# Optimization experiments

Hardware: AMD Instinct MI355X
Metric: run time of the kernel (lower is better)

## Reference

```python
import jax, jax.numpy as jnp
import numpy as np

B, S, D = 4, 2048, 1024
N_HEAD = 16
HEAD_DIM = D // N_HEAD


def setup_inputs() -> dict:
    key = jax.random.key(0)
    k1, k2, k3 = jax.random.split(key, 3)
    std = 0.02
    return {
        "x": jax.random.normal(k1, (B, S, D), dtype=jnp.float32),
        "c_attn_w": jax.random.normal(k2, (D, 3 * D), dtype=jnp.float32) * std,
        "c_attn_b": jnp.zeros((3 * D,), dtype=jnp.float32),
        "c_proj_w": jax.random.normal(k3, (D, D), dtype=jnp.float32) * std,
        "c_proj_b": jnp.zeros((D,), dtype=jnp.float32),
    }


def _split_heads(t):
    # [B, S, D] -> [B, H, S, hd]
    b, s, d = t.shape
    return t.reshape(b, s, N_HEAD, d // N_HEAD).transpose(0, 2, 1, 3)


def reference(x, c_attn_w, c_attn_b, c_proj_w, c_proj_b):
    # fused QKV projection (TFConv1D = x @ w + b)
    qkv = x @ c_attn_w + c_attn_b                      # [B, S, 3D]
    q, k, v = jnp.split(qkv, 3, axis=2)
    q, k, v = _split_heads(q), _split_heads(k), _split_heads(v)  # [B, H, S, hd]

    # scaled scores
    w = jnp.einsum('bhqd,bhkd->bhqk', q, k)
    w = w / jnp.sqrt(jnp.asarray(HEAD_DIM, w.dtype))

    # causal mask via multiplicative trick: i >= j - ns + nd (nd == ns == S)
    nd = ns = S
    i = jnp.arange(nd)[:, None]
    j = jnp.arange(ns)[None, :]
    b = (i >= j - ns + nd).astype(w.dtype)[None, None]  # [1,1,nd,ns]
    w = w * b - 10000.0 * (1.0 - b)

    w = jax.nn.softmax(w, axis=-1)
    a = jnp.einsum('bhqk,bhkd->bhqd', w, v)            # [B, H, S, hd]

    # merge heads: [B, H, S, hd] -> [B, S, D]
    a = a.transpose(0, 2, 1, 3).reshape(x.shape[0], x.shape[1], -1)
    a = a @ c_proj_w + c_proj_b
    return a
```

## Files before the change

### kernel.cpp

```cpp
#include <hip/hip_runtime.h>
#include <hip/hip_bf16.h>

typedef unsigned short ushort_t;
typedef __attribute__((ext_vector_type(8))) short short8;
typedef __attribute__((ext_vector_type(4))) float floatx4;

#define LOG2E 1.4426950408889634f

__device__ __forceinline__ unsigned short f2bf(float f) {
    unsigned u = __float_as_uint(f);
    u += 0x7FFF + ((u >> 16) & 1);
    return (unsigned short)(u >> 16);
}

__device__ __forceinline__ void async_ld16(const void* gptr, void* lptr) {
    typedef const __attribute__((address_space(1))) unsigned int TG;
    typedef __attribute__((address_space(3))) unsigned int TL;
    __builtin_amdgcn_global_load_lds((TG*)(unsigned long long)gptr,
                                     (TL*)(unsigned)(unsigned long long)lptr,
                                     16, 0, 0);
}

__global__ __launch_bounds__(256) void prep_kernel(const float* __restrict__ x,
                                                   const float* __restrict__ wqkv,
                                                   const float* __restrict__ wproj,
                                                   ushort_t* __restrict__ xb,
                                                   ushort_t* __restrict__ wqkvT,
                                                   ushort_t* __restrict__ wprojT) {
    __shared__ float t[32][33];
    int bx = blockIdx.x;
    if (bx < 8192) {
        int i = bx * 256 + threadIdx.x;
        float4 v = ((const float4*)x)[i];
        unsigned long long r = (unsigned long long)f2bf(v.x)
                             | ((unsigned long long)f2bf(v.y) << 16)
                             | ((unsigned long long)f2bf(v.z) << 32)
                             | ((unsigned long long)f2bf(v.w) << 48);
        ((unsigned long long*)xb)[i] = r;
        return;
    }
    const float* in; ushort_t* out; int R, C, bidx;
    if (bx < 8192 + 3072) { in = wqkv; out = wqkvT; R = 1024; C = 3072; bidx = bx - 8192; }
    else                  { in = wproj; out = wprojT; R = 1024; C = 1024; bidx = bx - 11264; }
    int nbc = C >> 5;
    int bc = bidx % nbc, br = bidx / nbc;
    int tx = threadIdx.x & 31, ty = threadIdx.x >> 5;
    int r0 = br << 5, c0 = bc << 5;
#pragma unroll
    for (int j = 0; j < 4; ++j)
        t[ty + j * 8][tx] = in[(size_t)(r0 + ty + j * 8) * C + c0 + tx];
    __syncthreads();
#pragma unroll
    for (int j = 0; j < 4; ++j)
        out[(size_t)(c0 + ty + j * 8) * R + r0 + tx] = f2bf(t[tx][ty + j * 8]);
}

__global__ __launch_bounds__(1024) void gemm_qkv_kernel(const ushort_t* __restrict__ A,
                                                        const ushort_t* __restrict__ Bt,
                                                        const float* __restrict__ bias,
                                                        ushort_t* __restrict__ qbuf,
                                                        ushort_t* __restrict__ kbuf,
                                                        ushort_t* __restrict__ vtbuf) {
    extern __shared__ __align__(16) ushort_t lds[];

    int bid = blockIdx.x;
    int wg = (bid & 7) * 96 + (bid >> 3);
    int bm = wg & 63, bn = wg >> 6;
    int m0 = bm << 7, n0 = bn << 8;

    int tid = threadIdx.x;
    int wave = tid >> 6, lane = tid & 63;
    int c = lane & 15, g = lane >> 4;
    int wm = wave >> 2, wn = wave & 3;

    int row0 = tid >> 3;
    int sch  = (tid & 7) ^ (row0 & 7);
    size_t aoff = (size_t)(m0 + row0) * 1024 + sch * 8;
    size_t boff = (size_t)(n0 + row0) * 1024 + sch * 8;

    int co0 = (g * 8) ^ ((c & 7) << 3);
    int co1 = co0 ^ 32;

    floatx4 acc[2][4];
    short8 a[2][2], bf[2][2], bg[2][2];
#pragma unroll
    for (int i2 = 0; i2 < 2; ++i2)
#pragma unroll
        for (int j2 = 0; j2 < 4; ++j2) { floatx4 z = {0.f,0.f,0.f,0.f}; acc[i2][j2] = z; }

    auto stA = [&](int t, int buf) {
        async_ld16(A + aoff + (size_t)t * 64, lds + buf * 8192 + tid * 8);
    };
    auto stB = [&](int t, int buf) {
        const ushort_t* s = Bt + boff + (size_t)t * 64;
        ushort_t* d = lds + 16384 + buf * 16384 + tid * 8;
        async_ld16(s, d);
        async_ld16(s + 131072, d + 8192);
    };
    auto ld_a = [&](int buf) {
#pragma unroll
        for (int mi = 0; mi < 2; ++mi) {
            int ro = buf * 8192 + (wm * 32 + mi * 16 + c) * 64;
            a[mi][0] = *(const short8*)&lds[ro + co0];
            a[mi][1] = *(const short8*)&lds[ro + co1];
        }
    };
    auto ld_b = [&](int buf, int q, short8 (&bb)[2][2]) {
#pragma unroll
        for (int nii = 0; nii < 2; ++nii) {
            int ro = 16384 + buf * 16384 + (wn * 64 + (q * 2 + nii) * 16 + c) * 64;
            bb[nii][0] = *(const short8*)&lds[ro + co0];
            bb[nii][1] = *(const short8*)&lds[ro + co1];
        }
    };
    auto phase_mm = [&](int q, short8 (&bb)[2][2]) {
        asm volatile("s_barrier" ::: "memory");
        asm volatile("s_waitcnt lgkmcnt(0)" ::: "memory");
        __builtin_amdgcn_s_setprio(1);
#pragma unroll
        for (int mi = 0; mi < 2; ++mi)
#pragma unroll
            for (int nii = 0; nii < 2; ++nii)
#pragma unroll
                for (int ks = 0; ks < 2; ++ks)
                    acc[mi][q * 2 + nii] =
                        __builtin_amdgcn_mfma_f32_16x16x32_bf16(
                            a[mi][ks], bb[nii][ks], acc[mi][q * 2 + nii], 0, 0, 0);
        __builtin_amdgcn_s_setprio(0);
        asm volatile("s_barrier" ::: "memory");
    };

    stA(0, 0); stB(0, 0);
    stA(1, 1); stB(1, 1);
    asm volatile("s_waitcnt vmcnt(3)" ::: "memory");
    asm volatile("s_barrier" ::: "memory");

#pragma unroll 1
    for (int i = 0; i < 14; ++i) {
        int buf = i & 1;
        ld_a(buf); ld_b(buf, 0, bf);
        stA(i + 2, buf);
        phase_mm(0, bf);
        ld_b(buf, 1, bg);
        stB(i + 2, buf);
        asm volatile("s_waitcnt vmcnt(3)" ::: "memory");
        phase_mm(1, bg);
    }
    ld_a(0); ld_b(0, 0, bf);
    phase_mm(0, bf);
    ld_b(0, 1, bg);
    asm volatile("s_waitcnt vmcnt(0)" ::: "memory");
    phase_mm(1, bg);
    ld_a(1); ld_b(1, 0, bf);
    phase_mm(0, bf);
    ld_b(1, 1, bg);
    phase_mm(1, bg);

    int sec = n0 >> 10;
    int h0 = (n0 & 1023) >> 6;
    int b  = m0 >> 11, sbase = m0 & 2047;
    int bh0 = b * 16 + h0;
    float bv[4];
#pragma unroll
    for (int ni = 0; ni < 4; ++ni) bv[ni] = bias[n0 + wn * 64 + ni * 16 + c];

    __syncthreads();

    if (sec < 2) {
        float scl = (sec == 0) ? (0.125f * LOG2E) : 1.0f;
#pragma unroll
        for (int mi = 0; mi < 2; ++mi)
#pragma unroll
            for (int ni = 0; ni < 4; ++ni)
#pragma unroll
                for (int r = 0; r < 4; ++r) {
                    int row = wm * 32 + mi * 16 + g * 4 + r;
                    lds[wn * 9216 + row * 72 + ni * 16 + c] =
                        f2bf((acc[mi][ni][r] + bv[ni]) * scl);
                }
        __syncthreads();
        ushort_t* dstbase = (sec == 0 ? qbuf : kbuf);
        int head = tid >> 8, row = (tid >> 1) & 127, half = tid & 1;
        const ushort_t* src = &lds[head * 9216 + row * 72 + half * 32];
        ushort_t* dst = dstbase + (size_t)(bh0 + head) * 131072
                      + (size_t)(sbase + row) * 64 + half * 32;
#pragma unroll
        for (int j = 0; j < 4; ++j)
            *(short8*)(dst + j * 8) = *(const short8*)(src + j * 8);
    } else {
#pragma unroll
        for (int mi = 0; mi < 2; ++mi)
#pragma unroll
            for (int ni = 0; ni < 4; ++ni) {
                int d = ni * 16 + c;
                int s0 = wm * 32 + mi * 16 + g * 4;
                unsigned long long pk =
                      (unsigned long long)f2bf(acc[mi][ni][0] + bv[ni])
                    | ((unsigned long long)f2bf(acc[mi][ni][1] + bv[ni]) << 16)
                    | ((unsigned long long)f2bf(acc[mi][ni][2] + bv[ni]) << 32)
                    | ((unsigned long long)f2bf(acc[mi][ni][3] + bv[ni]) << 48);
                *(unsigned long long*)&lds[wn * 8704 + d * 136 + s0] = pk;
            }
        __syncthreads();
        int head = tid >> 8, dd = (tid >> 2) & 63, sq = tid & 3;
        const ushort_t* src = &lds[head * 8704 + dd * 136 + sq * 32];
        ushort_t* dst = vtbuf + (size_t)(bh0 + head) * 131072
                      + (size_t)dd * 2048 + sbase + sq * 32;
#pragma unroll
        for (int j = 0; j < 4; ++j)
            *(short8*)(dst + j * 8) = *(const short8*)(src + j * 8);
    }
}

__global__ __launch_bounds__(256, 6) void attn_kernel(const ushort_t* __restrict__ qb_,
                                                      const ushort_t* __restrict__ kb_,
                                                      const ushort_t* __restrict__ vtb_,
                                                      ushort_t* __restrict__ aout) {
    __shared__ __align__(16) ushort_t Ks[64 * 68];
    __shared__ __align__(16) ushort_t Vs[64 * 68];
    __shared__ __align__(16) ushort_t Ps[4][16 * 68];
    int bx = blockIdx.x;
    int qb = 31 - (bx >> 6);
    int bhix = bx & 63;
    int b = bhix >> 4, h = bhix & 15;
    int q0 = qb << 6;
    int tid = threadIdx.x, wave = tid >> 6, lane = tid & 63;
    int c = lane & 15, g = lane >> 4;
    size_t bh = (size_t)(b * 16 + h);

    const ushort_t* Qp = qb_ + (bh * 2048 + q0) * 64;
    const ushort_t* Kp = kb_ + bh * 131072;
    const ushort_t* Vp = vtb_ + bh * 131072;

    int qr = wave * 16 + c;
    short8 qf0 = *(const short8*)(Qp + qr * 64 + g * 8);
    short8 qf1 = *(const short8*)(Qp + qr * 64 + 32 + g * 8);

    short8 vones;
#pragma unroll
    for (int j = 0; j < 8; ++j) vones[j] = (short)0x3F80;

    floatx4 o_acc[4];
    floatx4 lacc = {0.f, 0.f, 0.f, 0.f};
#pragma unroll
    for (int nt = 0; nt < 4; ++nt) { floatx4 z = {0.f,0.f,0.f,0.f}; o_acc[nt] = z; }

    short8 kreg[2], vreg[2];
#pragma unroll
    for (int it = 0; it < 2; ++it) {
        int idx = it * 256 + tid;
        kreg[it] = *(const short8*)(Kp + idx * 8);
        vreg[it] = *(const short8*)(Vp + (idx >> 3) * 2048 + (idx & 7) * 8);
    }

    int qg = q0 + wave * 16 + c;
    for (int kt = 0; kt <= qb; ++kt) {
        int kt0 = kt << 6;
        __syncthreads();
#pragma unroll
        for (int it = 0; it < 2; ++it) {
            int idx = it * 256 + tid;
            *(short8*)&Ks[(idx >> 3) * 68 + (idx & 7) * 8] = kreg[it];
            *(short8*)&Vs[(idx >> 3) * 68 + (idx & 7) * 8] = vreg[it];
        }
        __syncthreads();
        if (kt < qb) {
            int s0 = (kt + 1) << 6;
#pragma unroll
            for (int it = 0; it < 2; ++it) {
                int idx = it * 256 + tid;
                kreg[it] = *(const short8*)(Kp + s0 * 64 + idx * 8);
                vreg[it] = *(const short8*)(Vp + (idx >> 3) * 2048 + s0 + (idx & 7) * 8);
            }
        }
        bool diag = (kt == qb);

#pragma unroll
        for (int nt = 0; nt < 4; ++nt) {
            short8 kf0 = *(const short8*)&Ks[(nt * 16 + c) * 68 + g * 8];
            short8 kf1 = *(const short8*)&Ks[(nt * 16 + c) * 68 + 32 + g * 8];
            floatx4 z = {0.f, 0.f, 0.f, 0.f};
            z = __builtin_amdgcn_mfma_f32_16x16x32_bf16(kf0, qf0, z, 0, 0, 0);
            z = __builtin_amdgcn_mfma_f32_16x16x32_bf16(kf1, qf1, z, 0, 0, 0);

            int kpb = kt0 + nt * 16 + g * 4;
            float p[4];
#pragma unroll
            for (int r = 0; r < 4; ++r) {
                float s = z[r];
                if (diag) s = (kpb + r > qg) ? -1e30f : s;
                p[r] = exp2f(s);
            }
            union { unsigned long long u; __hip_bfloat162 h2[2]; } pk;
            pk.h2[0] = __float22bfloat162_rn(make_float2(p[0], p[1]));
            pk.h2[1] = __float22bfloat162_rn(make_float2(p[2], p[3]));
            *(unsigned long long*)&Ps[wave][c * 68 + nt * 16 + g * 4] = pk.u;
        }

#pragma unroll
        for (int ks = 0; ks < 2; ++ks) {
            short8 pf = *(const short8*)&Ps[wave][c * 68 + ks * 32 + g * 8];
            lacc = __builtin_amdgcn_mfma_f32_16x16x32_bf16(pf, vones, lacc, 0, 0, 0);
#pragma unroll
            for (int nt = 0; nt < 4; ++nt) {
                short8 vf = *(const short8*)&Vs[(nt * 16 + c) * 68 + ks * 32 + g * 8];
                o_acc[nt] = __builtin_amdgcn_mfma_f32_16x16x32_bf16(pf, vf, o_acc[nt], 0, 0, 0);
            }
        }
    }

    float inv[4];
#pragma unroll
    for (int r = 0; r < 4; ++r)
        inv[r] = 1.0f / lacc[r];
#pragma unroll
    for (int nt = 0; nt < 4; ++nt)
#pragma unroll
        for (int r = 0; r < 4; ++r) {
            int q = q0 + wave * 16 + g * 4 + r;
            aout[(size_t)(b * 2048 + q) * 1024 + h * 64 + nt * 16 + c] =
                f2bf(o_acc[nt][r] * inv[r]);
        }
}

__global__ __launch_bounds__(256) void gemm_proj_kernel(const ushort_t* __restrict__ A,
                                                        const ushort_t* __restrict__ Bt,
                                                        const float* __restrict__ bias,
                                                        float* __restrict__ Cout) {
    const int K = 1024, N = 1024, nbn = 8;
    __shared__ __align__(16) ushort_t As[128 * 32];
    __shared__ __align__(16) ushort_t Bs[128 * 32];
    int bm = blockIdx.x / nbn, bn = blockIdx.x % nbn;
    int m0 = bm << 7, n0 = bn << 7;
    int tid = threadIdx.x;
    int wave = tid >> 6, lane = tid & 63;
    int c = lane & 15, g = lane >> 4;
    int m_off = (wave & 1) << 6, n_off = (wave >> 1) << 6;
    int ldrow = lane >> 2;
    int ldk   = (lane & 3) << 3;

    floatx4 acc[4][4];
#pragma unroll
    for (int mi = 0; mi < 4; ++mi)
#pragma unroll
        for (int ni = 0; ni < 4; ++ni) {
            floatx4 z = {0.f, 0.f, 0.f, 0.f};
            acc[mi][ni] = z;
        }

    for (int kk = 0; kk < K; kk += 32) {
        __syncthreads();
#pragma unroll
        for (int j = 0; j < 2; ++j) {
            int chunk = wave * 2 + j;
            async_ld16(A  + (size_t)(m0 + chunk * 16 + ldrow) * K + kk + ldk, &As[chunk * 512]);
            async_ld16(Bt + (size_t)(n0 + chunk * 16 + ldrow) * K + kk + ldk, &Bs[chunk * 512]);
        }
        __syncthreads();
        short8 bf[4];
#pragma unroll
        for (int ni = 0; ni < 4; ++ni)
            bf[ni] = *(const short8*)&Bs[(n_off + ni * 16 + c) * 32 + g * 8];
#pragma unroll
        for (int mi = 0; mi < 4; ++mi) {
            short8 af = *(const short8*)&As[(m_off + mi * 16 + c) * 32 + g * 8];
#pragma unroll
            for (int ni = 0; ni < 4; ++ni)
                acc[mi][ni] = __builtin_amdgcn_mfma_f32_16x16x32_bf16(af, bf[ni], acc[mi][ni], 0, 0, 0);
        }
    }

    float bv[4];
#pragma unroll
    for (int ni = 0; ni < 4; ++ni) bv[ni] = bias[n0 + n_off + ni * 16 + c];
#pragma unroll
    for (int mi = 0; mi < 4; ++mi)
#pragma unroll
        for (int ni = 0; ni < 4; ++ni)
#pragma unroll
            for (int r = 0; r < 4; ++r) {
                int row = m0 + m_off + mi * 16 + g * 4 + r;
                int col = n0 + n_off + ni * 16 + c;
                Cout[(size_t)row * N + col] = acc[mi][ni][r] + bv[ni];
            }
}

extern "C" void kernel_launch(void* const* d_in, const int* in_sizes, int n_in,
                              void* d_out, int out_size, void* d_ws, size_t ws_size,
                              hipStream_t stream) {
    const float* x        = (const float*)d_in[0];
    const float* c_attn_w = (const float*)d_in[1];
    const float* c_attn_b = (const float*)d_in[2];
    const float* c_proj_w = (const float*)d_in[3];
    const float* c_proj_b = (const float*)d_in[4];
    float* out = (float*)d_out;

    char* ws = (char*)d_ws;
    ushort_t* xb     = (ushort_t*)(ws);
    ushort_t* wqkvT  = (ushort_t*)(ws + 16777216);
    ushort_t* wprojT = (ushort_t*)(ws + 23068672);
    ushort_t* qbuf   = (ushort_t*)(ws + 25165824);
    ushort_t* kbuf   = (ushort_t*)(ws + 41943040);
    ushort_t* vtbuf  = (ushort_t*)(ws + 58720256);

    static bool s_attr_set = false;
    if (!s_attr_set) {
        (void)hipFuncSetAttribute(reinterpret_cast<const void*>(gemm_qkv_kernel),
                                  hipFuncAttributeMaxDynamicSharedMemorySize, 98304);
        s_attr_set = true;
    }

    prep_kernel<<<12288, 256, 0, stream>>>(x, c_attn_w, c_proj_w, xb, wqkvT, wprojT);
    gemm_qkv_kernel<<<768, 1024, 98304, stream>>>(xb, wqkvT, c_attn_b, qbuf, kbuf, vtbuf);
    attn_kernel<<<2048, 256, 0, stream>>>(qbuf, kbuf, vtbuf, xb);
    gemm_proj_kernel<<<64 * 8, 256, 0, stream>>>(xb, wprojT, c_proj_b, out);
}
```

Measured before the change: 279.2 us.

## Widen QKV GEMM tiles to 128x384 and port proj GEMM to pipelined 1024-thread kernel

The QKV GEMM moves from 128x256 tiles with 768 blocks to 128x384 tiles with 512 blocks, giving each wave a 64x48 sub-tile. The epilogue now handles a block spanning up to six heads and mixed Q/K/V sections, writing them out per head. The output projection GEMM is replaced with the same double-buffered, swizzled, async-LDS 1024-thread design using 256x128 tiles. The aim is more reuse of each operand load per MFMA and better latency hiding in the projection. The cost is more LDS per block (128KB) and fewer blocks, which may reduce occupancy or leave CUs unevenly loaded.

Result: faster. 262.6 us (-5.9%).

```diff
diff --git a/kernel.cpp b/kernel.cpp
--- a/kernel.cpp
+++ b/kernel.cpp
@@ -64,14 +64,14 @@
     extern __shared__ __align__(16) ushort_t lds[];
 
     int bid = blockIdx.x;
-    int wg = (bid & 7) * 96 + (bid >> 3);
+    int wg = (bid & 7) * 64 + (bid >> 3);
     int bm = wg & 63, bn = wg >> 6;
-    int m0 = bm << 7, n0 = bn << 8;
+    int m0 = bm << 7, n0 = bn * 384;
 
     int tid = threadIdx.x;
     int wave = tid >> 6, lane = tid & 63;
     int c = lane & 15, g = lane >> 4;
-    int wm = wave >> 2, wn = wave & 3;
+    int wm = wave >> 3, wn = wave & 7;
 
     int row0 = tid >> 3;
     int sch  = (tid & 7) ^ (row0 & 7);
@@ -81,134 +81,139 @@
     int co0 = (g * 8) ^ ((c & 7) << 3);
     int co1 = co0 ^ 32;
 
-    floatx4 acc[2][4];
-    short8 a[2][2], bf[2][2], bg[2][2];
-#pragma unroll
-    for (int i2 = 0; i2 < 2; ++i2)
-#pragma unroll
-        for (int j2 = 0; j2 < 4; ++j2) { floatx4 z = {0.f,0.f,0.f,0.f}; acc[i2][j2] = z; }
+    floatx4 acc[4][3];
+    short8 a[4][2], bb[2];
+#pragma unroll
+    for (int i2 = 0; i2 < 4; ++i2)
+#pragma unroll
+        for (int j2 = 0; j2 < 3; ++j2) { floatx4 z = {0.f,0.f,0.f,0.f}; acc[i2][j2] = z; }
 
     auto stA = [&](int t, int buf) {
         async_ld16(A + aoff + (size_t)t * 64, lds + buf * 8192 + tid * 8);
     };
     auto stB = [&](int t, int buf) {
         const ushort_t* s = Bt + boff + (size_t)t * 64;
-        ushort_t* d = lds + 16384 + buf * 16384 + tid * 8;
+        ushort_t* d = lds + 16384 + buf * 24576 + tid * 8;
         async_ld16(s, d);
         async_ld16(s + 131072, d + 8192);
+        async_ld16(s + 262144, d + 16384);
     };
     auto ld_a = [&](int buf) {
 #pragma unroll
-        for (int mi = 0; mi < 2; ++mi) {
-            int ro = buf * 8192 + (wm * 32 + mi * 16 + c) * 64;
+        for (int mi = 0; mi < 4; ++mi) {
+            int ro = buf * 8192 + (wm * 64 + mi * 16 + c) * 64;
             a[mi][0] = *(const short8*)&lds[ro + co0];
             a[mi][1] = *(const short8*)&lds[ro + co1];
         }
     };
-    auto ld_b = [&](int buf, int q, short8 (&bb)[2][2]) {
-#pragma unroll
-        for (int nii = 0; nii < 2; ++nii) {
-            int ro = 16384 + buf * 16384 + (wn * 64 + (q * 2 + nii) * 16 + c) * 64;
-            bb[nii][0] = *(const short8*)&lds[ro + co0];
-            bb[nii][1] = *(const short8*)&lds[ro + co1];
-        }
-    };
-    auto phase_mm = [&](int q, short8 (&bb)[2][2]) {
+    auto ld_b = [&](int buf, int nii) {
+        int ro = 16384 + buf * 24576 + (wn * 48 + nii * 16 + c) * 64;
+        bb[0] = *(const short8*)&lds[ro + co0];
+        bb[1] = *(const short8*)&lds[ro + co1];
+    };
+    auto mm = [&](int nii) {
         asm volatile("s_barrier" ::: "memory");
         asm volatile("s_waitcnt lgkmcnt(0)" ::: "memory");
         __builtin_amdgcn_s_setprio(1);
 #pragma unroll
-        for (int mi = 0; mi < 2; ++mi)
-#pragma unroll
-            for (int nii = 0; nii < 2; ++nii)
-#pragma unroll
-                for (int ks = 0; ks < 2; ++ks)
-                    acc[mi][q * 2 + nii] =
-                        __builtin_amdgcn_mfma_f32_16x16x32_bf16(
-                            a[mi][ks], bb[nii][ks], acc[mi][q * 2 + nii], 0, 0, 0);
+        for (int mi = 0; mi < 4; ++mi)
+#pragma unroll
+            for (int ks = 0; ks < 2; ++ks)
+                acc[mi][nii] = __builtin_amdgcn_mfma_f32_16x16x32_bf16(
+                    a[mi][ks], bb[ks], acc[mi][nii], 0, 0, 0);
         __builtin_amdgcn_s_setprio(0);
         asm volatile("s_barrier" ::: "memory");
     };
 
     stA(0, 0); stB(0, 0);
     stA(1, 1); stB(1, 1);
-    asm volatile("s_waitcnt vmcnt(3)" ::: "memory");
+    asm volatile("s_waitcnt vmcnt(4)" ::: "memory");
     asm volatile("s_barrier" ::: "memory");
 
 #pragma unroll 1
-    for (int i = 0; i < 14; ++i) {
-        int buf = i & 1;
-        ld_a(buf); ld_b(buf, 0, bf);
-        stA(i + 2, buf);
-        phase_mm(0, bf);
-        ld_b(buf, 1, bg);
-        stB(i + 2, buf);
-        asm volatile("s_waitcnt vmcnt(3)" ::: "memory");
-        phase_mm(1, bg);
-    }
-    ld_a(0); ld_b(0, 0, bf);
-    phase_mm(0, bf);
-    ld_b(0, 1, bg);
+    for (int t = 0; t < 14; ++t) {
+        int buf = t & 1;
+        ld_a(buf); ld_b(buf, 0);
+        mm(0);
+        ld_b(buf, 1);
+        mm(1);
+        ld_b(buf, 2);
+        stA(t + 2, buf); stB(t + 2, buf);
+        asm volatile("s_waitcnt vmcnt(4)" ::: "memory");
+        mm(2);
+    }
+    ld_a(0); ld_b(0, 0);
+    mm(0);
+    ld_b(0, 1);
+    mm(1);
+    ld_b(0, 2);
     asm volatile("s_waitcnt vmcnt(0)" ::: "memory");
-    phase_mm(1, bg);
-    ld_a(1); ld_b(1, 0, bf);
-    phase_mm(0, bf);
-    ld_b(1, 1, bg);
-    phase_mm(1, bg);
-
-    int sec = n0 >> 10;
-    int h0 = (n0 & 1023) >> 6;
-    int b  = m0 >> 11, sbase = m0 & 2047;
-    int bh0 = b * 16 + h0;
-    float bv[4];
-#pragma unroll
-    for (int ni = 0; ni < 4; ++ni) bv[ni] = bias[n0 + wn * 64 + ni * 16 + c];
+    mm(2);
+    ld_a(1); ld_b(1, 0);
+    mm(0);
+    ld_b(1, 1);
+    mm(1);
+    ld_b(1, 2);
+    mm(2);
+
+    int b = m0 >> 11, sbase = m0 & 2047;
+    float bv[3], scl[3];
+    int headf[3], cinh[3], secf[3];
+#pragma unroll
+    for (int nii = 0; nii < 3; ++nii) {
+        int cb = wn * 48 + nii * 16;
+        bv[nii]   = bias[n0 + cb + c];
+        headf[nii] = cb >> 6;
+        cinh[nii]  = (cb & 63) + c;
+        secf[nii]  = (n0 + cb) >> 10;
+        scl[nii]   = (secf[nii] == 0) ? (0.125f * LOG2E) : 1.0f;
+    }
 
     __syncthreads();
 
-    if (sec < 2) {
-        float scl = (sec == 0) ? (0.125f * LOG2E) : 1.0f;
-#pragma unroll
-        for (int mi = 0; mi < 2; ++mi)
-#pragma unroll
-            for (int ni = 0; ni < 4; ++ni)
+#pragma unroll
+    for (int nii = 0; nii < 3; ++nii) {
+        if (secf[nii] < 2) {
+#pragma unroll
+            for (int mi = 0; mi < 4; ++mi)
 #pragma unroll
                 for (int r = 0; r < 4; ++r) {
-                    int row = wm * 32 + mi * 16 + g * 4 + r;
-                    lds[wn * 9216 + row * 72 + ni * 16 + c] =
-                        f2bf((acc[mi][ni][r] + bv[ni]) * scl);
+                    int row = wm * 64 + mi * 16 + g * 4 + r;
+                    lds[headf[nii] * 9216 + row * 72 + cinh[nii]] =
+                        f2bf((acc[mi][nii][r] + bv[nii]) * scl[nii]);
                 }
-        __syncthreads();
-        ushort_t* dstbase = (sec == 0 ? qbuf : kbuf);
-        int head = tid >> 8, row = (tid >> 1) & 127, half = tid & 1;
-        const ushort_t* src = &lds[head * 9216 + row * 72 + half * 32];
-        ushort_t* dst = dstbase + (size_t)(bh0 + head) * 131072
-                      + (size_t)(sbase + row) * 64 + half * 32;
-#pragma unroll
-        for (int j = 0; j < 4; ++j)
-            *(short8*)(dst + j * 8) = *(const short8*)(src + j * 8);
-    } else {
-#pragma unroll
-        for (int mi = 0; mi < 2; ++mi)
-#pragma unroll
-            for (int ni = 0; ni < 4; ++ni) {
-                int d = ni * 16 + c;
-                int s0 = wm * 32 + mi * 16 + g * 4;
+        } else {
+#pragma unroll
+            for (int mi = 0; mi < 4; ++mi) {
+                int d = cinh[nii];
+                int s0 = wm * 64 + mi * 16 + g * 4;
                 unsigned long long pk =
-                      (unsigned long long)f2bf(acc[mi][ni][0] + bv[ni])
-                    | ((unsigned long long)f2bf(acc[mi][ni][1] + bv[ni]) << 16)
-                    | ((unsigned long long)f2bf(acc[mi][ni][2] + bv[ni]) << 32)
-                    | ((unsigned long long)f2bf(acc[mi][ni][3] + bv[ni]) << 48);
-                *(unsigned long long*)&lds[wn * 8704 + d * 136 + s0] = pk;
+                      (unsigned long long)f2bf(acc[mi][nii][0] + bv[nii])
+                    | ((unsigned long long)f2bf(acc[mi][nii][1] + bv[nii]) << 16)
+                    | ((unsigned long long)f2bf(acc[mi][nii][2] + bv[nii]) << 32)
+                    | ((unsigned long long)f2bf(acc[mi][nii][3] + bv[nii]) << 48);
+                *(unsigned long long*)&lds[headf[nii] * 9216 + d * 136 + s0] = pk;
             }
-        __syncthreads();
-        int head = tid >> 8, dd = (tid >> 2) & 63, sq = tid & 3;
-        const ushort_t* src = &lds[head * 8704 + dd * 136 + sq * 32];
-        ushort_t* dst = vtbuf + (size_t)(bh0 + head) * 131072
-                      + (size_t)dd * 2048 + sbase + sq * 32;
-#pragma unroll
-        for (int j = 0; j < 4; ++j)
-            *(short8*)(dst + j * 8) = *(const short8*)(src + j * 8);
+        }
+    }
+    __syncthreads();
+
+#pragma unroll 1
+    for (int hl = 0; hl < 6; ++hl) {
+        int colg = n0 + hl * 64;
+        int sech = colg >> 10;
+        int hg = (colg & 1023) >> 6;
+        size_t bh = (size_t)(b * 16 + hg);
+        if (sech < 2) {
+            int row = tid >> 3, ch = tid & 7;
+            ushort_t* dst = (sech == 0 ? qbuf : kbuf) + bh * 131072
+                          + (size_t)(sbase + row) * 64 + ch * 8;
+            *(short8*)dst = *(const short8*)&lds[hl * 9216 + row * 72 + ch * 8];
+        } else {
+            int d = tid >> 4, sq = tid & 15;
+            ushort_t* dst = vtbuf + bh * 131072 + (size_t)d * 2048 + sbase + sq * 8;
+            *(short8*)dst = *(const short8*)&lds[hl * 9216 + d * 136 + sq * 8];
+        }
     }
 }
 
@@ -323,65 +328,110 @@
         }
 }
 
-__global__ __launch_bounds__(256) void gemm_proj_kernel(const ushort_t* __restrict__ A,
-                                                        const ushort_t* __restrict__ Bt,
-                                                        const float* __restrict__ bias,
-                                                        float* __restrict__ Cout) {
-    const int K = 1024, N = 1024, nbn = 8;
-    __shared__ __align__(16) ushort_t As[128 * 32];
-    __shared__ __align__(16) ushort_t Bs[128 * 32];
-    int bm = blockIdx.x / nbn, bn = blockIdx.x % nbn;
-    int m0 = bm << 7, n0 = bn << 7;
+__global__ __launch_bounds__(1024) void gemm_proj_kernel(const ushort_t* __restrict__ A,
+                                                         const ushort_t* __restrict__ Bt,
+                                                         const float* __restrict__ bias,
+                                                         float* __restrict__ Cout) {
+    extern __shared__ __align__(16) ushort_t lds[];
+
+    int bid = blockIdx.x;
+    int wg = (bid & 7) * 32 + (bid >> 3);
+    int bm = wg & 31, bn = wg >> 5;
+    int m0 = bm << 8, n0 = bn << 7;
+
     int tid = threadIdx.x;
     int wave = tid >> 6, lane = tid & 63;
     int c = lane & 15, g = lane >> 4;
-    int m_off = (wave & 1) << 6, n_off = (wave >> 1) << 6;
-    int ldrow = lane >> 2;
-    int ldk   = (lane & 3) << 3;
-
-    floatx4 acc[4][4];
+    int wm = wave >> 2, wn = wave & 3;
+
+    int row0 = tid >> 3;
+    int sch  = (tid & 7) ^ (row0 & 7);
+    size_t aoff = (size_t)(m0 + row0) * 1024 + sch * 8;
+    size_t boff = (size_t)(n0 + row0) * 1024 + sch * 8;
+
+    int co0 = (g * 8) ^ ((c & 7) << 3);
+    int co1 = co0 ^ 32;
+
+    floatx4 acc[4][2];
+    short8 a[4][2], bb[2];
+#pragma unroll
+    for (int i2 = 0; i2 < 4; ++i2)
+#pragma unroll
+        for (int j2 = 0; j2 < 2; ++j2) { floatx4 z = {0.f,0.f,0.f,0.f}; acc[i2][j2] = z; }
+
+    auto stA = [&](int t, int buf) {
+        const ushort_t* s = A + aoff + (size_t)t * 64;
+        ushort_t* d = lds + buf * 16384 + tid * 8;
+        async_ld16(s, d);
+        async_ld16(s + 131072, d + 8192);
+    };
+    auto stB = [&](int t, int buf) {
+        async_ld16(Bt + boff + (size_t)t * 64, lds + 32768 + buf * 8192 + tid * 8);
+    };
+    auto ld_a = [&](int buf) {
+#pragma unroll
+        for (int mi = 0; mi < 4; ++mi) {
+            int ro = buf * 16384 + (wm * 64 + mi * 16 + c) * 64;
+            a[mi][0] = *(const short8*)&lds[ro + co0];
+            a[mi][1] = *(const short8*)&lds[ro + co1];
+        }
+    };
+    auto ld_b = [&](int buf, int nii) {
+        int ro = 32768 + buf * 8192 + (wn * 32 + nii * 16 + c) * 64;
+        bb[0] = *(const short8*)&lds[ro + co0];
+        bb[1] = *(const short8*)&lds[ro + co1];
+    };
+    auto mm = [&](int nii) {
+        asm volatile("s_barrier" ::: "memory");
+        asm volatile("s_waitcnt lgkmcnt(0)" ::: "memory");
+        __builtin_amdgcn_s_setprio(1);
+#pragma unroll
+        for (int mi = 0; mi < 4; ++mi)
+#pragma unroll
+            for (int ks = 0; ks < 2; ++ks)
+                acc[mi][nii] = __builtin_amdgcn_mfma_f32_16x16x32_bf16(
+                    a[mi][ks], bb[ks], acc[mi][nii], 0, 0, 0);
+        __builtin_amdgcn_s_setprio(0);
+        asm volatile("s_barrier" ::: "memory");
+    };
+
+    stA(0, 0); stB(0, 0);
+    stA(1, 1); stB(1, 1);
+    asm volatile("s_waitcnt vmcnt(3)" ::: "memory");
+    asm volatile("s_barrier" ::: "memory");
+
+#pragma unroll 1
+    for (int t = 0; t < 14; ++t) {
+        int buf = t & 1;
+        ld_a(buf); ld_b(buf, 0);
+        mm(0);
+        ld_b(buf, 1);
+        stA(t + 2, buf); stB(t + 2, buf);
+        asm volatile("s_waitcnt vmcnt(3)" ::: "memory");
+        mm(1);
+    }
+    ld_a(0); ld_b(0, 0);
+    mm(0);
+    ld_b(0, 1);
+    asm volatile("s_waitcnt vmcnt(0)" ::: "memory");
+    mm(1);
+    ld_a(1); ld_b(1, 0);
+    mm(0);
+    ld_b(1, 1);
+    mm(1);
+
+    float bv[2];
+#pragma unroll
+    for (int nii = 0; nii < 2; ++nii) bv[nii] = bias[n0 + wn * 32 + nii * 16 + c];
 #pragma unroll
     for (int mi = 0; mi < 4; ++mi)
 #pragma unroll
-        for (int ni = 0; ni < 4; ++ni) {
-            floatx4 z = {0.f, 0.f, 0.f, 0.f};
-            acc[mi][ni] = z;
-        }
-
-    for (int kk = 0; kk < K; kk += 32) {
-        __syncthreads();
-#pragma unroll
-        for (int j = 0; j < 2; ++j) {
-            int chunk = wave * 2 + j;
-            async_ld16(A  + (size_t)(m0 + chunk * 16 + ldrow) * K + kk + ldk, &As[chunk * 512]);
-            async_ld16(Bt + (size_t)(n0 + chunk * 16 + ldrow) * K + kk + ldk, &Bs[chunk * 512]);
-        }
-        __syncthreads();
-        short8 bf[4];
-#pragma unroll
-        for (int ni = 0; ni < 4; ++ni)
-            bf[ni] = *(const short8*)&Bs[(n_off + ni * 16 + c) * 32 + g * 8];
-#pragma unroll
-        for (int mi = 0; mi < 4; ++mi) {
-            short8 af = *(const short8*)&As[(m_off + mi * 16 + c) * 32 + g * 8];
-#pragma unroll
-            for (int ni = 0; ni < 4; ++ni)
-                acc[mi][ni] = __builtin_amdgcn_mfma_f32_16x16x32_bf16(af, bf[ni], acc[mi][ni], 0, 0, 0);
-        }
-    }
-
-    float bv[4];
-#pragma unroll
-    for (int ni = 0; ni < 4; ++ni) bv[ni] = bias[n0 + n_off + ni * 16 + c];
-#pragma unroll
-    for (int mi = 0; mi < 4; ++mi)
-#pragma unroll
-        for (int ni = 0; ni < 4; ++ni)
+        for (int nii = 0; nii < 2; ++nii)
 #pragma unroll
             for (int r = 0; r < 4; ++r) {
-                int row = m0 + m_off + mi * 16 + g * 4 + r;
-                int col = n0 + n_off + ni * 16 + c;
-                Cout[(size_t)row * N + col] = acc[mi][ni][r] + bv[ni];
+                int row = m0 + wm * 64 + mi * 16 + g * 4 + r;
+                int col = n0 + wn * 32 + nii * 16 + c;
+                Cout[(size_t)row * 1024 + col] = acc[mi][nii][r] + bv[nii];
             }
 }
 
@@ -406,12 +456,14 @@
     static bool s_attr_set = false;
     if (!s_attr_set) {
         (void)hipFuncSetAttribute(reinterpret_cast<const void*>(gemm_qkv_kernel),
+                                  hipFuncAttributeMaxDynamicSharedMemorySize, 131072);
+        (void)hipFuncSetAttribute(reinterpret_cast<const void*>(gemm_proj_kernel),
                                   hipFuncAttributeMaxDynamicSharedMemorySize, 98304);
         s_attr_set = true;
     }
 
     prep_kernel<<<12288, 256, 0, stream>>>(x, c_attn_w, c_proj_w, xb, wqkvT, wprojT);
-    gemm_qkv_kernel<<<768, 1024, 98304, stream>>>(xb, wqkvT, c_attn_b, qbuf, kbuf, vtbuf);
+    gemm_qkv_kernel<<<512, 1024, 131072, stream>>>(xb, wqkvT, c_attn_b, qbuf, kbuf, vtbuf);
     attn_kernel<<<2048, 256, 0, stream>>>(qbuf, kbuf, vtbuf, xb);
-    gemm_proj_kernel<<<64 * 8, 256, 0, stream>>>(xb, wprojT, c_proj_b, out);
-}
+    gemm_proj_kernel<<<256, 1024, 98304, stream>>>(xb, wprojT, c_proj_b, out);
+}
```
